# Kernel optimization log

Measured on AMD Instinct MI355X. Metric: run time of the kernel, lower is better.

## Reference

```python
import jax, jax.numpy as jnp
import numpy as np
import math

N_HEAD = 16
N_EMBD = 1024
HEAD_DIM = N_EMBD // N_HEAD
B, S = 2, 2048


def apply_rope(x):
    # x: [B, H, S, d]
    seq_len, d_k = x.shape[-2], x.shape[-1]
    half = d_k // 2
    inv_freq = 1.0 / (10000.0 ** (jnp.arange(half, dtype=jnp.float32) / half))
    ang = jnp.arange(seq_len, dtype=jnp.float32)[:, None] * inv_freq[None, :]  # [S, half]
    sin, cos = jnp.sin(ang), jnp.cos(ang)
    x1, x2 = x[..., :half], x[..., half:]
    return jnp.concatenate([x1 * cos - x2 * sin, x1 * sin + x2 * cos], axis=-1)


def _proj(x, W):
    # torch Linear: y = x @ W^T ; reshape to heads: [B, S, E] -> [B, H, S, d]
    b, s, _ = x.shape
    y = jnp.einsum('bse,fe->bsf', x, W)
    return y.reshape(b, s, N_HEAD, HEAD_DIM).transpose(0, 2, 1, 3)


def _attention(Q, K, V, mask, scale):
    scores = jnp.einsum('bhqd,bhkd->bhqk', Q, K) * scale
    scores = jnp.where(mask == 0, jnp.float32(-1e9), scores)
    w = jax.nn.softmax(scores, axis=-1)
    ctx = jnp.einsum('bhqk,bhkd->bhqd', w, V)
    return ctx, w


def setup_inputs() -> dict:
    key = jax.random.key(0)
    ks = jax.random.split(key, 10)
    std = 0.02
    inp = {
        'query': jax.random.normal(ks[0], (B, S, N_EMBD), jnp.float32),
        'key': jax.random.normal(ks[1], (B, S, N_EMBD), jnp.float32),
        'value': jax.random.normal(ks[2], (B, S, N_EMBD), jnp.float32),
        'mask': jnp.tril(jnp.ones((S, S), dtype=bool))[None, None],  # causal [1,1,S,S]
        'WQ1': std * jax.random.normal(ks[3], (N_EMBD, N_EMBD), jnp.float32),
        'WK1': std * jax.random.normal(ks[4], (N_EMBD, N_EMBD), jnp.float32),
        'WV1': std * jax.random.normal(ks[5], (N_EMBD, N_EMBD), jnp.float32),
        'WQ2': std * jax.random.normal(ks[6], (N_EMBD, N_EMBD), jnp.float32),
        'WK2': std * jax.random.normal(ks[7], (N_EMBD, N_EMBD), jnp.float32),
        'WV2': std * jax.random.normal(ks[8], (N_EMBD, N_EMBD), jnp.float32),
        'WO': std * jax.random.normal(ks[9], (N_EMBD, N_EMBD), jnp.float32),
    }
    return inp


def reference(query, key, value, mask, WQ1, WK1, WV1, WQ2, WK2, WV2, WO):
    scale = 1.0 / math.sqrt(HEAD_DIM)
    Q1 = apply_rope(_proj(query, WQ1))
    K1 = apply_rope(_proj(key, WK1))
    V1 = _proj(value, WV1)
    Q2 = apply_rope(_proj(query, WQ2))
    K2 = apply_rope(_proj(key, WK2))
    V2 = _proj(value, WV2)
    ctx1, w1 = _attention(Q1, K1, V1, mask, scale)
    ctx2, w2 = _attention(Q2, K2, V2, mask, scale)
    ctx = ctx1 * ctx2  # elementwise fusion of the two attention paths
    b, h, s, d = ctx.shape
    ctx = ctx.transpose(0, 2, 1, 3).reshape(b, s, h * d)
    out = jnp.einsum('bse,fe->bsf', ctx, WO)
    return out, w1, w2
```

## Files before the change

kernel.cpp:

```cpp
#include <hip/hip_runtime.h>
#include <hip/hip_bf16.h>
#include <math.h>

#define S_LEN 2048
#define NHEAD 16
#define HDIM 64
#define EMB 1024
#define NBATCH 2
#define MROWS (NBATCH * S_LEN)
#define BH 32
#define QKV_T ((size_t)BH * S_LEN * HDIM)
#define W_ELEMS ((size_t)S_LEN * S_LEN * BH)
#define OUT_ELEMS ((size_t)MROWS * EMB)

typedef __bf16 bf16x8 __attribute__((ext_vector_type(8)));
typedef float f32x4 __attribute__((ext_vector_type(4)));

__device__ inline unsigned short f2bf(float f) {
    unsigned int u = __float_as_uint(f);
    unsigned int r = (u + 0x7fffu + ((u >> 16) & 1u)) >> 16;
    return (unsigned short)r;
}

__global__ __launch_bounds__(256) void conv_all_k(const float* __restrict__ s0, const float* __restrict__ s1,
                                                  const float* __restrict__ s2, const float* __restrict__ s3,
                                                  const float* __restrict__ s4, const float* __restrict__ s5,
                                                  const float* __restrict__ s6, const float* __restrict__ s7,
                                                  const float* __restrict__ s8, const float* __restrict__ s9,
                                                  unsigned short* __restrict__ qb, unsigned short* __restrict__ kb,
                                                  unsigned short* __restrict__ vb, unsigned short* __restrict__ wb) {
    int t = blockIdx.y;
    const float* src;
    unsigned short* dst;
    int n4;
    if (t < 3) {
        src = t == 0 ? s0 : (t == 1 ? s1 : s2);
        dst = t == 0 ? qb : (t == 1 ? kb : vb);
        n4 = (int)(OUT_ELEMS / 4);
    } else {
        const float* ws[7] = {s3, s4, s5, s6, s7, s8, s9};
        src = ws[t - 3];
        dst = wb + (size_t)(t - 3) * EMB * EMB;
        n4 = (EMB * EMB) / 4;
    }
    int i = blockIdx.x * 256 + threadIdx.x;
    if (i < n4) {
        float4 v = ((const float4*)src)[i];
        ushort4 o;
        o.x = f2bf(v.x); o.y = f2bf(v.y); o.z = f2bf(v.z); o.w = f2bf(v.w);
        ((ushort4*)dst)[i] = o;
    }
}

__global__ __launch_bounds__(256) void gemm_proj_k(const unsigned short* __restrict__ qb,
                                                   const unsigned short* __restrict__ kb,
                                                   const unsigned short* __restrict__ vb,
                                                   const unsigned short* __restrict__ wb,
                                                   unsigned short* __restrict__ qkv) {
    __shared__ unsigned short As[128][72];
    __shared__ unsigned short Bs[128][72];
    int g = blockIdx.z;
    int sel = g % 3;
    const unsigned short* X = sel == 0 ? qb : (sel == 1 ? kb : vb);
    const unsigned short* W = wb + (size_t)g * (EMB * EMB);
    unsigned short* Y = qkv + (size_t)g * QKV_T;
    bool rope = sel < 2;

    int bm = blockIdx.y, bn = blockIdx.x;
    int tid = threadIdx.x;
    int wid = tid >> 6, lane = tid & 63;
    int wm = wid >> 1, wn = wid & 1;
    int col = lane & 15, quad = lane >> 4;

    f32x4 acc[4][4] = {};

    for (int k0 = 0; k0 < EMB; k0 += 64) {
        int4 ar[4], br[4];
#pragma unroll
        for (int c = 0; c < 4; c++) {
            int cid = c * 256 + tid;
            int row = cid >> 3, cc = (cid & 7) * 8;
            ar[c] = *(const int4*)(X + (size_t)(bm * 128 + row) * EMB + k0 + cc);
            br[c] = *(const int4*)(W + (size_t)(bn * 128 + row) * EMB + k0 + cc);
        }
        __syncthreads();
#pragma unroll
        for (int c = 0; c < 4; c++) {
            int cid = c * 256 + tid;
            int row = cid >> 3, cc = (cid & 7) * 8;
            *(int4*)(&As[row][cc]) = ar[c];
            *(int4*)(&Bs[row][cc]) = br[c];
        }
        __syncthreads();
#pragma unroll
        for (int kk = 0; kk < 64; kk += 32) {
            bf16x8 af[4], bf[4];
#pragma unroll
            for (int i = 0; i < 4; i++)
                af[i] = *(const bf16x8*)(&As[wm * 64 + i * 16 + col][kk + quad * 8]);
#pragma unroll
            for (int i = 0; i < 4; i++)
                bf[i] = *(const bf16x8*)(&Bs[wn * 64 + i * 16 + col][kk + quad * 8]);
#pragma unroll
            for (int i = 0; i < 4; i++)
#pragma unroll
                for (int j = 0; j < 4; j++)
                    acc[i][j] = __builtin_amdgcn_mfma_f32_16x16x32_bf16(af[i], bf[j], acc[i][j], 0, 0, 0);
        }
        __syncthreads();
    }

    int h = bn * 2 + wn;
#pragma unroll
    for (int mi = 0; mi < 4; mi++) {
#pragma unroll
        for (int r = 0; r < 4; r++) {
            int m = bm * 128 + wm * 64 + mi * 16 + quad * 4 + r;
            int b = m >> 11, s = m & (S_LEN - 1);
            unsigned short* Yrow = Y + ((size_t)(b * NHEAD + h) * S_LEN + s) * HDIM;
            if (rope) {
#pragma unroll
                for (int ni = 0; ni < 2; ni++) {
                    int d1 = ni * 16 + col;
                    float x1 = acc[mi][ni][r];
                    float x2 = acc[mi][ni + 2][r];
                    float inv_freq = powf(10000.f, -(float)d1 * (1.0f / 32.0f));
                    float ang = (float)s * inv_freq;
                    float sn, cs;
                    sincosf(ang, &sn, &cs);
                    Yrow[d1] = f2bf(x1 * cs - x2 * sn);
                    Yrow[d1 + 32] = f2bf(x1 * sn + x2 * cs);
                }
            } else {
#pragma unroll
                for (int ni = 0; ni < 4; ni++)
                    Yrow[ni * 16 + col] = f2bf(acc[mi][ni][r]);
            }
        }
    }
}

__global__ __launch_bounds__(256) void vtrans_k(const unsigned short* __restrict__ qkv,
                                                unsigned short* __restrict__ vt) {
    __shared__ unsigned short t[64][65];
    int copy = blockIdx.z, bh = blockIdx.y;
    int s0 = blockIdx.x * 64;
    const unsigned short* V = qkv + (size_t)(copy * 3 + 2) * QKV_T + (size_t)bh * S_LEN * HDIM;
    unsigned short* VT = vt + (size_t)copy * QKV_T + (size_t)bh * HDIM * S_LEN;
    int tid = threadIdx.x;
#pragma unroll
    for (int c = 0; c < 16; c++) {
        int idx = c * 256 + tid;
        int sl = idx >> 6, d = idx & 63;
        t[sl][d] = V[(size_t)(s0 + sl) * HDIM + d];
    }
    __syncthreads();
#pragma unroll
    for (int c = 0; c < 16; c++) {
        int idx = c * 256 + tid;
        int dl = idx >> 6, sl = idx & 63;
        VT[(size_t)dl * S_LEN + s0 + sl] = t[sl][dl];
    }
}

__global__ __launch_bounds__(512) void attn_fused_k(const unsigned short* __restrict__ qkv,
                                                    const unsigned short* __restrict__ vt,
                                                    float* __restrict__ wout_base,
                                                    unsigned short* __restrict__ ctxp) {
    __shared__ unsigned short P[8][2][16][40];

    int d = blockIdx.x;
    int xcd = d & 7;
    int idx = d >> 3;
    int bh = (xcd << 2) | (idx >> 4);
    int pair = idx & 15;

    int b = bh >> 4, h = bh & 15;
    int wid = threadIdx.x >> 6, lane = threadIdx.x & 63;
    int sub = wid & 3;
    int qt = (wid < 4) ? pair : (31 - pair);
    int col = lane & 15, quad = lane >> 4;
    int q0 = qt * 64 + sub * 16;

    const unsigned short* Q1 = qkv + (size_t)bh * S_LEN * HDIM;
    const unsigned short* K1 = qkv + QKV_T + (size_t)bh * S_LEN * HDIM;
    const unsigned short* Q2 = qkv + 3 * QKV_T + (size_t)bh * S_LEN * HDIM;
    const unsigned short* K2 = qkv + 4 * QKV_T + (size_t)bh * S_LEN * HDIM;
    const unsigned short* VT1 = vt + (size_t)bh * HDIM * S_LEN;
    const unsigned short* VT2 = vt + QKV_T + (size_t)bh * HDIM * S_LEN;
    float* W1 = wout_base + (size_t)bh * S_LEN * S_LEN;
    float* W2 = wout_base + W_ELEMS + (size_t)bh * S_LEN * S_LEN;

    const unsigned short* qr1 = Q1 + (size_t)(q0 + col) * HDIM;
    bf16x8 a10 = *(const bf16x8*)(qr1 + quad * 8);
    bf16x8 a11 = *(const bf16x8*)(qr1 + 32 + quad * 8);
    const unsigned short* qr2 = Q2 + (size_t)(q0 + col) * HDIM;
    bf16x8 a20 = *(const bf16x8*)(qr2 + quad * 8);
    bf16x8 a21 = *(const bf16x8*)(qr2 + 32 + quad * 8);

    int ktmaxw = qt * 4 + sub;
    const float NEG = -1e30f;
    float m1[4] = {NEG, NEG, NEG, NEG}, l1[4] = {0.f, 0.f, 0.f, 0.f};
    float m2[4] = {NEG, NEG, NEG, NEG}, l2[4] = {0.f, 0.f, 0.f, 0.f};

    for (int kt = 0; kt <= ktmaxw; kt++) {
        const unsigned short* kr1 = K1 + (size_t)(kt * 16 + col) * HDIM;
        bf16x8 b10 = *(const bf16x8*)(kr1 + quad * 8);
        bf16x8 b11 = *(const bf16x8*)(kr1 + 32 + quad * 8);
        f32x4 c1 = {};
        c1 = __builtin_amdgcn_mfma_f32_16x16x32_bf16(a10, b10, c1, 0, 0, 0);
        c1 = __builtin_amdgcn_mfma_f32_16x16x32_bf16(a11, b11, c1, 0, 0, 0);
        const unsigned short* kr2 = K2 + (size_t)(kt * 16 + col) * HDIM;
        bf16x8 b20 = *(const bf16x8*)(kr2 + quad * 8);
        bf16x8 b21 = *(const bf16x8*)(kr2 + 32 + quad * 8);
        f32x4 c2 = {};
        c2 = __builtin_amdgcn_mfma_f32_16x16x32_bf16(a20, b20, c2, 0, 0, 0);
        c2 = __builtin_amdgcn_mfma_f32_16x16x32_bf16(a21, b21, c2, 0, 0, 0);
        int kg = kt * 16 + col;
#pragma unroll
        for (int r = 0; r < 4; r++) {
            int qg = q0 + quad * 4 + r;
            if (kg <= qg) {
                float s1 = c1[r] * 0.125f;
                float mn1 = fmaxf(m1[r], s1);
                l1[r] = l1[r] * __expf(m1[r] - mn1) + __expf(s1 - mn1);
                m1[r] = mn1;
                float s2 = c2[r] * 0.125f;
                float mn2 = fmaxf(m2[r], s2);
                l2[r] = l2[r] * __expf(m2[r] - mn2) + __expf(s2 - mn2);
                m2[r] = mn2;
            }
        }
    }
    float mr1[4], il1[4], mr2[4], il2[4];
#pragma unroll
    for (int r = 0; r < 4; r++) {
        float m = m1[r], l = l1[r];
#pragma unroll
        for (int off = 1; off < 16; off <<= 1) {
            float mo = __shfl_xor(m, off);
            float lo = __shfl_xor(l, off);
            float mn = fmaxf(m, mo);
            l = l * __expf(m - mn) + lo * __expf(mo - mn);
            m = mn;
        }
        mr1[r] = m; il1[r] = 1.f / l;
        m = m2[r]; l = l2[r];
#pragma unroll
        for (int off = 1; off < 16; off <<= 1) {
            float mo = __shfl_xor(m, off);
            float lo = __shfl_xor(l, off);
            float mn = fmaxf(m, mo);
            l = l * __expf(m - mn) + lo * __expf(mo - mn);
            m = mn;
        }
        mr2[r] = m; il2[r] = 1.f / l;
    }

    f32x4 acc1[4] = {}, acc2[4] = {};
    int pvmax = qt * 2 + (sub >> 1);
    for (int kt2 = 0; kt2 <= pvmax; kt2++) {
#pragma unroll
        for (int s2i = 0; s2i < 2; s2i++) {
            int kt = kt2 * 2 + s2i;
            float wv1[4], wv2[4];
            if (kt <= ktmaxw) {
                const unsigned short* kr1 = K1 + (size_t)(kt * 16 + col) * HDIM;
                bf16x8 b10 = *(const bf16x8*)(kr1 + quad * 8);
                bf16x8 b11 = *(const bf16x8*)(kr1 + 32 + quad * 8);
                f32x4 c1 = {};
                c1 = __builtin_amdgcn_mfma_f32_16x16x32_bf16(a10, b10, c1, 0, 0, 0);
                c1 = __builtin_amdgcn_mfma_f32_16x16x32_bf16(a11, b11, c1, 0, 0, 0);
                const unsigned short* kr2 = K2 + (size_t)(kt * 16 + col) * HDIM;
                bf16x8 b20 = *(const bf16x8*)(kr2 + quad * 8);
                bf16x8 b21 = *(const bf16x8*)(kr2 + 32 + quad * 8);
                f32x4 c2 = {};
                c2 = __builtin_amdgcn_mfma_f32_16x16x32_bf16(a20, b20, c2, 0, 0, 0);
                c2 = __builtin_amdgcn_mfma_f32_16x16x32_bf16(a21, b21, c2, 0, 0, 0);
                int kg = kt * 16 + col;
#pragma unroll
                for (int r = 0; r < 4; r++) {
                    int qg = q0 + quad * 4 + r;
                    wv1[r] = (kg <= qg) ? __expf(c1[r] * 0.125f - mr1[r]) * il1[r] : 0.f;
                    wv2[r] = (kg <= qg) ? __expf(c2[r] * 0.125f - mr2[r]) * il2[r] : 0.f;
                }
            } else {
#pragma unroll
                for (int r = 0; r < 4; r++) { wv1[r] = 0.f; wv2[r] = 0.f; }
            }
            int kgc = kt * 16 + col;
#pragma unroll
            for (int r = 0; r < 4; r++) {
                int qg = q0 + quad * 4 + r;
                __builtin_nontemporal_store(wv1[r], &W1[(size_t)qg * S_LEN + kgc]);
                __builtin_nontemporal_store(wv2[r], &W2[(size_t)qg * S_LEN + kgc]);
                P[wid][0][quad * 4 + r][s2i * 16 + col] = f2bf(wv1[r]);
                P[wid][1][quad * 4 + r][s2i * 16 + col] = f2bf(wv2[r]);
            }
        }
        bf16x8 pa1 = *(const bf16x8*)(&P[wid][0][col][quad * 8]);
        bf16x8 pa2 = *(const bf16x8*)(&P[wid][1][col][quad * 8]);
#pragma unroll
        for (int ni = 0; ni < 4; ni++) {
            bf16x8 bv1 = *(const bf16x8*)(VT1 + (size_t)(ni * 16 + col) * S_LEN + kt2 * 32 + quad * 8);
            acc1[ni] = __builtin_amdgcn_mfma_f32_16x16x32_bf16(pa1, bv1, acc1[ni], 0, 0, 0);
            bf16x8 bv2 = *(const bf16x8*)(VT2 + (size_t)(ni * 16 + col) * S_LEN + kt2 * 32 + quad * 8);
            acc2[ni] = __builtin_amdgcn_mfma_f32_16x16x32_bf16(pa2, bv2, acc2[ni], 0, 0, 0);
        }
    }

    int z4 = (pvmax + 1) * 8;
#pragma unroll 1
    for (int r = 0; r < 16; r++) {
        float* row1 = W1 + (size_t)(q0 + r) * S_LEN;
        float* row2 = W2 + (size_t)(q0 + r) * S_LEN;
        f32x4 z = {0.f, 0.f, 0.f, 0.f};
        for (int c4 = z4 + lane; c4 < 512; c4 += 64) {
            __builtin_nontemporal_store(z, (f32x4*)row1 + c4);
            __builtin_nontemporal_store(z, (f32x4*)row2 + c4);
        }
    }

#pragma unroll
    for (int ni = 0; ni < 4; ni++)
#pragma unroll
        for (int r = 0; r < 4; r++) {
            int qg = q0 + quad * 4 + r;
            float v = acc1[ni][r] * acc2[ni][r];
            ctxp[((size_t)(b * S_LEN + qg)) * EMB + h * HDIM + ni * 16 + col] = f2bf(v);
        }
}

__global__ __launch_bounds__(256) void gemm_out_k(const unsigned short* __restrict__ A,
                                                  const unsigned short* __restrict__ W,
                                                  float* __restrict__ out) {
    __shared__ unsigned short As[128][72];
    __shared__ unsigned short Bs[128][72];
    int bm = blockIdx.y, bn = blockIdx.x;
    int tid = threadIdx.x;
    int wid = tid >> 6, lane = tid & 63;
    int wm = wid >> 1, wn = wid & 1;
    int col = lane & 15, quad = lane >> 4;

    f32x4 acc[4][4] = {};

    for (int k0 = 0; k0 < EMB; k0 += 64) {
        int4 ar[4], br[4];
#pragma unroll
        for (int c = 0; c < 4; c++) {
            int cid = c * 256 + tid;
            int row = cid >> 3, cc = (cid & 7) * 8;
            ar[c] = *(const int4*)(A + (size_t)(bm * 128 + row) * EMB + k0 + cc);
            br[c] = *(const int4*)(W + (size_t)(bn * 128 + row) * EMB + k0 + cc);
        }
        __syncthreads();
#pragma unroll
        for (int c = 0; c < 4; c++) {
            int cid = c * 256 + tid;
            int row = cid >> 3, cc = (cid & 7) * 8;
            *(int4*)(&As[row][cc]) = ar[c];
            *(int4*)(&Bs[row][cc]) = br[c];
        }
        __syncthreads();
#pragma unroll
        for (int kk = 0; kk < 64; kk += 32) {
            bf16x8 af[4], bf[4];
#pragma unroll
            for (int i = 0; i < 4; i++)
                af[i] = *(const bf16x8*)(&As[wm * 64 + i * 16 + col][kk + quad * 8]);
#pragma unroll
            for (int i = 0; i < 4; i++)
                bf[i] = *(const bf16x8*)(&Bs[wn * 64 + i * 16 + col][kk + quad * 8]);
#pragma unroll
            for (int i = 0; i < 4; i++)
#pragma unroll
                for (int j = 0; j < 4; j++)
                    acc[i][j] = __builtin_amdgcn_mfma_f32_16x16x32_bf16(af[i], bf[j], acc[i][j], 0, 0, 0);
        }
        __syncthreads();
    }
#pragma unroll
    for (int mi = 0; mi < 4; mi++)
#pragma unroll
        for (int ni = 0; ni < 4; ni++)
#pragma unroll
            for (int r = 0; r < 4; r++) {
                int m = bm * 128 + wm * 64 + mi * 16 + quad * 4 + r;
                int n = bn * 128 + wn * 64 + ni * 16 + col;
                out[(size_t)m * EMB + n] = acc[mi][ni][r];
            }
}

extern "C" void kernel_launch(void* const* d_in, const int* in_sizes, int n_in,
                              void* d_out, int out_size, void* d_ws, size_t ws_size,
                              hipStream_t stream) {
    const float* q = (const float*)d_in[0];
    const float* k = (const float*)d_in[1];
    const float* v = (const float*)d_in[2];

    char* ws = (char*)d_ws;
    size_t off = 0;
    auto alloc = [&](size_t bytes) -> void* {
        void* p = ws + off;
        off += (bytes + 255) & ~(size_t)255;
        return p;
    };
    unsigned short* qb = (unsigned short*)alloc(OUT_ELEMS * 2);
    unsigned short* kb = (unsigned short*)alloc(OUT_ELEMS * 2);
    unsigned short* vb = (unsigned short*)alloc(OUT_ELEMS * 2);
    unsigned short* wb = (unsigned short*)alloc((size_t)7 * EMB * EMB * 2);
    unsigned short* qkv = (unsigned short*)alloc((size_t)6 * QKV_T * 2);
    unsigned short* vt = (unsigned short*)alloc((size_t)2 * QKV_T * 2);
    unsigned short* ctxp = (unsigned short*)alloc(OUT_ELEMS * 2);

    conv_all_k<<<dim3(4096, 10), 256, 0, stream>>>(
        q, k, v, (const float*)d_in[4], (const float*)d_in[5], (const float*)d_in[6],
        (const float*)d_in[7], (const float*)d_in[8], (const float*)d_in[9],
        (const float*)d_in[10], qb, kb, vb, wb);

    gemm_proj_k<<<dim3(8, 32, 6), 256, 0, stream>>>(qb, kb, vb, wb, qkv);
    vtrans_k<<<dim3(32, 32, 2), 256, 0, stream>>>(qkv, vt);

    float* wout = (float*)d_out + OUT_ELEMS;
    attn_fused_k<<<dim3(512), dim3(512), 0, stream>>>(qkv, vt, wout, ctxp);

    gemm_out_k<<<dim3(8, 32), 256, 0, stream>>>(ctxp, wb + (size_t)6 * EMB * EMB, (float*)d_out);
}
```

Before: 1.709 ms.

## Split attention blocks per query tile, prefetch K and V tiles, raise MFMA priority

The attention kernel now runs 1024 blocks of 4 waves, one query tile each, heaviest tiles first, instead of 512 blocks that paired a light and a heavy tile. The statistics pass prefetches the next K tile while computing the current one. The PV pass issues all K and V^T loads up front before the softmax and MFMA work, and wraps the PV MFMAs in s_setprio. The aim is to hide global load latency and balance work across CUs, at the cost of more live registers and dropping the explicit pairing of tiles.

Result: slower. 1.768 ms (+3.4%).

```diff
diff --git a/kernel.cpp b/kernel.cpp
--- a/kernel.cpp
+++ b/kernel.cpp
@@ -163,22 +163,21 @@
     }
 }
 
-__global__ __launch_bounds__(512) void attn_fused_k(const unsigned short* __restrict__ qkv,
+__global__ __launch_bounds__(256) void attn_fused_k(const unsigned short* __restrict__ qkv,
                                                     const unsigned short* __restrict__ vt,
                                                     float* __restrict__ wout_base,
                                                     unsigned short* __restrict__ ctxp) {
-    __shared__ unsigned short P[8][2][16][40];
+    __shared__ unsigned short P[4][2][16][40];
 
     int d = blockIdx.x;
     int xcd = d & 7;
     int idx = d >> 3;
-    int bh = (xcd << 2) | (idx >> 4);
-    int pair = idx & 15;
+    int bh = (xcd << 2) | (idx >> 5);
+    int qt = 31 - (idx & 31);
 
     int b = bh >> 4, h = bh & 15;
     int wid = threadIdx.x >> 6, lane = threadIdx.x & 63;
-    int sub = wid & 3;
-    int qt = (wid < 4) ? pair : (31 - pair);
+    int sub = wid;
     int col = lane & 15, quad = lane >> 4;
     int q0 = qt * 64 + sub * 16;
 
@@ -203,19 +202,31 @@
     float m1[4] = {NEG, NEG, NEG, NEG}, l1[4] = {0.f, 0.f, 0.f, 0.f};
     float m2[4] = {NEG, NEG, NEG, NEG}, l2[4] = {0.f, 0.f, 0.f, 0.f};
 
+    bf16x8 k10, k11, k20, k21;
+    {
+        const unsigned short* kr1 = K1 + (size_t)col * HDIM;
+        k10 = *(const bf16x8*)(kr1 + quad * 8);
+        k11 = *(const bf16x8*)(kr1 + 32 + quad * 8);
+        const unsigned short* kr2 = K2 + (size_t)col * HDIM;
+        k20 = *(const bf16x8*)(kr2 + quad * 8);
+        k21 = *(const bf16x8*)(kr2 + 32 + quad * 8);
+    }
     for (int kt = 0; kt <= ktmaxw; kt++) {
-        const unsigned short* kr1 = K1 + (size_t)(kt * 16 + col) * HDIM;
-        bf16x8 b10 = *(const bf16x8*)(kr1 + quad * 8);
-        bf16x8 b11 = *(const bf16x8*)(kr1 + 32 + quad * 8);
+        bf16x8 c10 = k10, c11 = k11, c20 = k20, c21 = k21;
+        if (kt < ktmaxw) {
+            const unsigned short* kr1 = K1 + (size_t)((kt + 1) * 16 + col) * HDIM;
+            k10 = *(const bf16x8*)(kr1 + quad * 8);
+            k11 = *(const bf16x8*)(kr1 + 32 + quad * 8);
+            const unsigned short* kr2 = K2 + (size_t)((kt + 1) * 16 + col) * HDIM;
+            k20 = *(const bf16x8*)(kr2 + quad * 8);
+            k21 = *(const bf16x8*)(kr2 + 32 + quad * 8);
+        }
         f32x4 c1 = {};
-        c1 = __builtin_amdgcn_mfma_f32_16x16x32_bf16(a10, b10, c1, 0, 0, 0);
-        c1 = __builtin_amdgcn_mfma_f32_16x16x32_bf16(a11, b11, c1, 0, 0, 0);
-        const unsigned short* kr2 = K2 + (size_t)(kt * 16 + col) * HDIM;
-        bf16x8 b20 = *(const bf16x8*)(kr2 + quad * 8);
-        bf16x8 b21 = *(const bf16x8*)(kr2 + 32 + quad * 8);
+        c1 = __builtin_amdgcn_mfma_f32_16x16x32_bf16(a10, c10, c1, 0, 0, 0);
+        c1 = __builtin_amdgcn_mfma_f32_16x16x32_bf16(a11, c11, c1, 0, 0, 0);
         f32x4 c2 = {};
-        c2 = __builtin_amdgcn_mfma_f32_16x16x32_bf16(a20, b20, c2, 0, 0, 0);
-        c2 = __builtin_amdgcn_mfma_f32_16x16x32_bf16(a21, b21, c2, 0, 0, 0);
+        c2 = __builtin_amdgcn_mfma_f32_16x16x32_bf16(a20, c20, c2, 0, 0, 0);
+        c2 = __builtin_amdgcn_mfma_f32_16x16x32_bf16(a21, c21, c2, 0, 0, 0);
         int kg = kt * 16 + col;
 #pragma unroll
         for (int r = 0; r < 4; r++) {
@@ -260,53 +271,76 @@
     f32x4 acc1[4] = {}, acc2[4] = {};
     int pvmax = qt * 2 + (sub >> 1);
     for (int kt2 = 0; kt2 <= pvmax; kt2++) {
-#pragma unroll
-        for (int s2i = 0; s2i < 2; s2i++) {
-            int kt = kt2 * 2 + s2i;
-            float wv1[4], wv2[4];
-            if (kt <= ktmaxw) {
-                const unsigned short* kr1 = K1 + (size_t)(kt * 16 + col) * HDIM;
-                bf16x8 b10 = *(const bf16x8*)(kr1 + quad * 8);
-                bf16x8 b11 = *(const bf16x8*)(kr1 + 32 + quad * 8);
-                f32x4 c1 = {};
-                c1 = __builtin_amdgcn_mfma_f32_16x16x32_bf16(a10, b10, c1, 0, 0, 0);
-                c1 = __builtin_amdgcn_mfma_f32_16x16x32_bf16(a11, b11, c1, 0, 0, 0);
-                const unsigned short* kr2 = K2 + (size_t)(kt * 16 + col) * HDIM;
-                bf16x8 b20 = *(const bf16x8*)(kr2 + quad * 8);
-                bf16x8 b21 = *(const bf16x8*)(kr2 + 32 + quad * 8);
-                f32x4 c2 = {};
-                c2 = __builtin_amdgcn_mfma_f32_16x16x32_bf16(a20, b20, c2, 0, 0, 0);
-                c2 = __builtin_amdgcn_mfma_f32_16x16x32_bf16(a21, b21, c2, 0, 0, 0);
-                int kg = kt * 16 + col;
-#pragma unroll
-                for (int r = 0; r < 4; r++) {
-                    int qg = q0 + quad * 4 + r;
-                    wv1[r] = (kg <= qg) ? __expf(c1[r] * 0.125f - mr1[r]) * il1[r] : 0.f;
-                    wv2[r] = (kg <= qg) ? __expf(c2[r] * 0.125f - mr2[r]) * il2[r] : 0.f;
-                }
-            } else {
-#pragma unroll
-                for (int r = 0; r < 4; r++) { wv1[r] = 0.f; wv2[r] = 0.f; }
-            }
-            int kgc = kt * 16 + col;
+        int kt0 = kt2 * 2, kt1 = kt0 + 1;
+        const unsigned short* kr1 = K1 + (size_t)(kt0 * 16 + col) * HDIM;
+        bf16x8 b10 = *(const bf16x8*)(kr1 + quad * 8);
+        bf16x8 b11 = *(const bf16x8*)(kr1 + 32 + quad * 8);
+        const unsigned short* kr2 = K2 + (size_t)(kt0 * 16 + col) * HDIM;
+        bf16x8 b20 = *(const bf16x8*)(kr2 + quad * 8);
+        bf16x8 b21 = *(const bf16x8*)(kr2 + 32 + quad * 8);
+        f32x4 c1 = {}, c2 = {};
+        c1 = __builtin_amdgcn_mfma_f32_16x16x32_bf16(a10, b10, c1, 0, 0, 0);
+        c1 = __builtin_amdgcn_mfma_f32_16x16x32_bf16(a11, b11, c1, 0, 0, 0);
+        c2 = __builtin_amdgcn_mfma_f32_16x16x32_bf16(a20, b20, c2, 0, 0, 0);
+        c2 = __builtin_amdgcn_mfma_f32_16x16x32_bf16(a21, b21, c2, 0, 0, 0);
+        bool s1v = (kt1 <= ktmaxw);
+        bf16x8 d10 = {}, d11 = {}, d20 = {}, d21 = {};
+        if (s1v) {
+            const unsigned short* er1 = K1 + (size_t)(kt1 * 16 + col) * HDIM;
+            d10 = *(const bf16x8*)(er1 + quad * 8);
+            d11 = *(const bf16x8*)(er1 + 32 + quad * 8);
+            const unsigned short* er2 = K2 + (size_t)(kt1 * 16 + col) * HDIM;
+            d20 = *(const bf16x8*)(er2 + quad * 8);
+            d21 = *(const bf16x8*)(er2 + 32 + quad * 8);
+        }
+        bf16x8 bv1[4], bv2[4];
+#pragma unroll
+        for (int ni = 0; ni < 4; ni++) {
+            bv1[ni] = *(const bf16x8*)(VT1 + (size_t)(ni * 16 + col) * S_LEN + kt2 * 32 + quad * 8);
+            bv2[ni] = *(const bf16x8*)(VT2 + (size_t)(ni * 16 + col) * S_LEN + kt2 * 32 + quad * 8);
+        }
+        {
+            int kg = kt0 * 16 + col;
 #pragma unroll
             for (int r = 0; r < 4; r++) {
                 int qg = q0 + quad * 4 + r;
-                __builtin_nontemporal_store(wv1[r], &W1[(size_t)qg * S_LEN + kgc]);
-                __builtin_nontemporal_store(wv2[r], &W2[(size_t)qg * S_LEN + kgc]);
-                P[wid][0][quad * 4 + r][s2i * 16 + col] = f2bf(wv1[r]);
-                P[wid][1][quad * 4 + r][s2i * 16 + col] = f2bf(wv2[r]);
+                float w1v = (kg <= qg) ? __expf(c1[r] * 0.125f - mr1[r]) * il1[r] : 0.f;
+                float w2v = (kg <= qg) ? __expf(c2[r] * 0.125f - mr2[r]) * il2[r] : 0.f;
+                __builtin_nontemporal_store(w1v, &W1[(size_t)qg * S_LEN + kg]);
+                __builtin_nontemporal_store(w2v, &W2[(size_t)qg * S_LEN + kg]);
+                P[wid][0][quad * 4 + r][col] = f2bf(w1v);
+                P[wid][1][quad * 4 + r][col] = f2bf(w2v);
+            }
+        }
+        {
+            f32x4 e1 = {}, e2 = {};
+            if (s1v) {
+                e1 = __builtin_amdgcn_mfma_f32_16x16x32_bf16(a10, d10, e1, 0, 0, 0);
+                e1 = __builtin_amdgcn_mfma_f32_16x16x32_bf16(a11, d11, e1, 0, 0, 0);
+                e2 = __builtin_amdgcn_mfma_f32_16x16x32_bf16(a20, d20, e2, 0, 0, 0);
+                e2 = __builtin_amdgcn_mfma_f32_16x16x32_bf16(a21, d21, e2, 0, 0, 0);
+            }
+            int kg = kt1 * 16 + col;
+#pragma unroll
+            for (int r = 0; r < 4; r++) {
+                int qg = q0 + quad * 4 + r;
+                float w1v = (s1v && kg <= qg) ? __expf(e1[r] * 0.125f - mr1[r]) * il1[r] : 0.f;
+                float w2v = (s1v && kg <= qg) ? __expf(e2[r] * 0.125f - mr2[r]) * il2[r] : 0.f;
+                __builtin_nontemporal_store(w1v, &W1[(size_t)qg * S_LEN + kg]);
+                __builtin_nontemporal_store(w2v, &W2[(size_t)qg * S_LEN + kg]);
+                P[wid][0][quad * 4 + r][16 + col] = f2bf(w1v);
+                P[wid][1][quad * 4 + r][16 + col] = f2bf(w2v);
             }
         }
         bf16x8 pa1 = *(const bf16x8*)(&P[wid][0][col][quad * 8]);
         bf16x8 pa2 = *(const bf16x8*)(&P[wid][1][col][quad * 8]);
+        __builtin_amdgcn_s_setprio(1);
 #pragma unroll
         for (int ni = 0; ni < 4; ni++) {
-            bf16x8 bv1 = *(const bf16x8*)(VT1 + (size_t)(ni * 16 + col) * S_LEN + kt2 * 32 + quad * 8);
-            acc1[ni] = __builtin_amdgcn_mfma_f32_16x16x32_bf16(pa1, bv1, acc1[ni], 0, 0, 0);
-            bf16x8 bv2 = *(const bf16x8*)(VT2 + (size_t)(ni * 16 + col) * S_LEN + kt2 * 32 + quad * 8);
-            acc2[ni] = __builtin_amdgcn_mfma_f32_16x16x32_bf16(pa2, bv2, acc2[ni], 0, 0, 0);
-        }
+            acc1[ni] = __builtin_amdgcn_mfma_f32_16x16x32_bf16(pa1, bv1[ni], acc1[ni], 0, 0, 0);
+            acc2[ni] = __builtin_amdgcn_mfma_f32_16x16x32_bf16(pa2, bv2[ni], acc2[ni], 0, 0, 0);
+        }
+        __builtin_amdgcn_s_setprio(0);
     }
 
     int z4 = (pvmax + 1) * 8;
@@ -422,7 +456,7 @@
     vtrans_k<<<dim3(32, 32, 2), 256, 0, stream>>>(qkv, vt);
 
     float* wout = (float*)d_out + OUT_ELEMS;
-    attn_fused_k<<<dim3(512), dim3(512), 0, stream>>>(qkv, vt, wout, ctxp);
+    attn_fused_k<<<dim3(1024), dim3(256), 0, stream>>>(qkv, vt, wout, ctxp);
 
     gemm_out_k<<<dim3(8, 32), 256, 0, stream>>>(ctxp, wb + (size_t)6 * EMB * EMB, (float*)d_out);
 }
```
